# Kernel tuning notes

Hardware: AMD Instinct MI355X
Metric: run time of the kernel (lower is better)

Reference implementation:

```python
import jax, jax.numpy as jnp
import numpy as np

TAU = 2.0
EPS = 1e-5
T, B, C, H, W = 4, 16, 256, 32, 32
HEADS = 8
HD = C // HEADS
N = H * W


def make_spike(grad_fn):
    @jax.custom_vjp
    def f(x):
        return (x >= 0.0).astype(x.dtype)
    def fwd(x):
        return f(x), x
    def bwd(res, g):
        return (g * grad_fn(res),)
    f.defvjp(fwd, bwd)
    return f

# ATan surrogate (alpha=5.0) used by q/k/v LIF nodes
spike_atan5 = make_spike(lambda x: (5.0 / 2.0) / (1.0 + (jnp.pi / 2.0 * 5.0 * x) ** 2))
# default Sigmoid surrogate (alpha=4.0) for shortcut_lif / talking_heads_lif
def _sig_grad(x):
    s = jax.nn.sigmoid(4.0 * x)
    return 4.0 * s * (1.0 - s)
spike_sig4 = make_spike(_sig_grad)


def lif(x, spike, v_th=1.0):
    # multi-step LIF over leading time axis; hard reset to 0, detach_reset
    def step(v, xt):
        h = v + (xt - v) / TAU
        s = spike(h - v_th)
        v_new = h * (1.0 - jax.lax.stop_gradient(s))
        return v_new, s
    _, out = jax.lax.scan(step, jnp.zeros_like(x[0]), x)
    return out


def conv1x1(x, w):
    # x: (T,B,C,H,W), w: (Cout,Cin) from Conv2d kernel_size=1
    return jnp.einsum('tbchw,oc->tbohw', x, w)


def bn(y, gamma, beta, mean, var):
    scale = (gamma / jnp.sqrt(var + EPS))[None, None, :, None, None]
    shift = (beta - mean * gamma / jnp.sqrt(var + EPS))[None, None, :, None, None]
    return y * scale + shift


def to_heads(x):
    # (T,B,C,H,W) -> (T,B,heads,N,hd); matches flatten(3).transpose(-1,-2).reshape.permute
    x = x.reshape(T, B, C, N).transpose(0, 1, 3, 2)          # (T,B,N,C)
    x = x.reshape(T, B, N, HEADS, HD).transpose(0, 1, 3, 2, 4)  # (T,B,heads,N,hd)
    return x


def setup_inputs() -> dict:
    key = jax.random.key(0)
    ks = jax.random.split(key, 20)
    def bn_params(i):
        return (1.0 + 0.1 * jax.random.normal(ks[i], (C,), jnp.float32),
                0.1 * jax.random.normal(ks[i + 1], (C,), jnp.float32),
                0.1 * jax.random.normal(ks[i + 2], (C,), jnp.float32),
                jax.random.uniform(ks[i + 3], (C,), jnp.float32, 0.5, 1.5))
    q_g, q_b, q_m, q_var = bn_params(1)
    k_g, k_b, k_m, k_var = bn_params(5)
    v_g, v_b, v_m, v_var = bn_params(9)
    p_g, p_b, p_m, p_var = bn_params(13)
    std = 1.0 / np.sqrt(C)
    return {
        'x': jax.random.normal(ks[0], (T, B, C, H, W), jnp.float32),
        'q_w': std * jax.random.normal(ks[17], (C, C), jnp.float32),
        'q_g': q_g, 'q_b': q_b, 'q_m': q_m, 'q_var': q_var,
        'k_w': std * jax.random.normal(ks[18], (C, C), jnp.float32),
        'k_g': k_g, 'k_b': k_b, 'k_m': k_m, 'k_var': k_var,
        'v_w': std * jax.random.normal(ks[19], (C, C), jnp.float32),
        'v_g': v_g, 'v_b': v_b, 'v_m': v_m, 'v_var': v_var,
        'proj_w': std * jax.random.normal(ks[4], (C, C), jnp.float32),
        'proj_bias': 0.01 * jax.random.normal(ks[8], (C,), jnp.float32),
        'p_g': p_g, 'p_b': p_b, 'p_m': p_m, 'p_var': p_var,
    }


def reference(x, q_w, q_g, q_b, q_m, q_var, k_w, k_g, k_b, k_m, k_var,
              v_w, v_g, v_b, v_m, v_var, proj_w, proj_bias, p_g, p_b, p_m, p_var):
    identity = x
    xs = lif(x, spike_sig4, 1.0)                      # shortcut_lif
    q = to_heads(lif(bn(conv1x1(xs, q_w), q_g, q_b, q_m, q_var), spike_atan5, 1.0))
    k = to_heads(lif(bn(conv1x1(xs, k_w), k_g, k_b, k_m, k_var), spike_atan5, 1.0))
    v = to_heads(lif(bn(conv1x1(xs, v_w), v_g, v_b, v_m, v_var), spike_atan5, 1.0))
    kv = jnp.sum(k * v, axis=-2, keepdims=True)       # (T,B,heads,1,hd)
    kv = lif(kv, spike_sig4, 0.5)                     # talking_heads_lif, v_th=0.5
    attn = q * kv                                     # (T,B,heads,N,hd)
    # transpose(3,4).reshape(T,B,C,H,W)
    out = attn.transpose(0, 1, 2, 4, 3).reshape(T, B, C, H, W)
    out = conv1x1(out, proj_w) + proj_bias[None, None, :, None, None]
    out = bn(out, p_g, p_b, p_m, p_var)
    out = out + identity
    return out, v
```

## Files before the change

kernel.cpp:

```cpp
#include <hip/hip_runtime.h>
#include <hip/hip_bf16.h>
#include <stdint.h>

#define T_ 4
#define B_ 16
#define C_ 256
#define N_ 1024
#define HEADS_ 8
#define HD_ 32

typedef unsigned long long u64;
typedef unsigned char u8;

__global__ __launch_bounds__(256) void prep_transpose(
    const float* __restrict__ qw, const float* __restrict__ kw,
    const float* __restrict__ vw, const float* __restrict__ pw,
    float* __restrict__ wtq, float* __restrict__ wtk,
    float* __restrict__ wtv, float* __restrict__ wtp) {
  int c = blockIdx.x;
  int o = threadIdx.x;
  wtq[c * C_ + o] = qw[o * C_ + c];
  wtk[c * C_ + o] = kw[o * C_ + c];
  wtv[c * C_ + o] = vw[o * C_ + c];
  wtp[c * C_ + o] = pw[o * C_ + c];
}

__global__ __launch_bounds__(256) void prep_bn(
    const float* __restrict__ qg, const float* __restrict__ qb2,
    const float* __restrict__ qmn, const float* __restrict__ qvr,
    const float* __restrict__ kg, const float* __restrict__ kb2,
    const float* __restrict__ kmn, const float* __restrict__ kvr,
    const float* __restrict__ vg, const float* __restrict__ vb2,
    const float* __restrict__ vmn, const float* __restrict__ vvr,
    const float* __restrict__ pg, const float* __restrict__ pb2,
    const float* __restrict__ pmn, const float* __restrict__ pvr,
    float* __restrict__ bnt) {
  int c = threadIdx.x;
  float rs;
  rs = sqrtf(qvr[c] + 1e-5f);
  bnt[0 * C_ + c] = qg[c] / rs;
  bnt[1 * C_ + c] = qb2[c] - qmn[c] * qg[c] / rs;
  rs = sqrtf(kvr[c] + 1e-5f);
  bnt[2 * C_ + c] = kg[c] / rs;
  bnt[3 * C_ + c] = kb2[c] - kmn[c] * kg[c] / rs;
  rs = sqrtf(vvr[c] + 1e-5f);
  bnt[4 * C_ + c] = vg[c] / rs;
  bnt[5 * C_ + c] = vb2[c] - vmn[c] * vg[c] / rs;
  rs = sqrtf(pvr[c] + 1e-5f);
  bnt[6 * C_ + c] = pg[c] / rs;
  bnt[7 * C_ + c] = pb2[c] - pmn[c] * pg[c] / rs;
}

__global__ __launch_bounds__(256) void lif_shortcut(const float* __restrict__ x,
                                                    u64* __restrict__ xsm) {
  int b = blockIdx.x >> 5;
  int n0 = (blockIdx.x & 31) << 5;
  int tid = threadIdx.x;
  int l = tid & 63, w = tid >> 6;
  __shared__ float tile[C_ * 33];
  float v[32];
#pragma unroll
  for (int i = 0; i < 32; i++) v[i] = 0.f;
  int c = (w << 6) + l;
  for (int t = 0; t < T_; t++) {
    __syncthreads();
    const float* xp = x + (((size_t)t * B_ + b) * C_) * N_ + n0;
    for (int idx = tid; idx < C_ * 32; idx += 256) {
      int cc = idx >> 5, nn = idx & 31;
      tile[cc * 33 + nn] = xp[(size_t)cc * N_ + nn];
    }
    __syncthreads();
#pragma unroll
    for (int nn = 0; nn < 32; nn++) {
      float xv = tile[c * 33 + nn];
      float h = v[nn] + (xv - v[nn]) * 0.5f;
      bool s = h >= 1.0f;
      v[nn] = s ? 0.f : h;
      u64 bal = __ballot(s);
      if (l == nn) xsm[(((size_t)t * B_ + b) * N_ + n0 + nn) * 4 + w] = bal;
    }
  }
}

__global__ __launch_bounds__(256) void qkv_sparse(
    const u64* __restrict__ xsm,
    const float* __restrict__ wtq, const float* __restrict__ wtk,
    const float* __restrict__ wtv, const float* __restrict__ bnt,
    float* __restrict__ pkv, u64* __restrict__ qm_out,
    float* __restrict__ vout) {
  int b = blockIdx.x >> 6;
  int nt = blockIdx.x & 63;
  int n0 = nt << 4;
  int tid = threadIdx.x;
  int l = tid & 63, wv = tid >> 6;
  float qs[4], qsh[4], ks[4], ksh[4], vsc[4], vsh[4];
#pragma unroll
  for (int j = 0; j < 4; j++) {
    int o = (j << 6) + l;
    qs[j]  = bnt[0 * C_ + o]; qsh[j] = bnt[1 * C_ + o];
    ks[j]  = bnt[2 * C_ + o]; ksh[j] = bnt[3 * C_ + o];
    vsc[j] = bnt[4 * C_ + o]; vsh[j] = bnt[5 * C_ + o];
  }
  int cnt[4][4];
#pragma unroll
  for (int t = 0; t < 4; t++)
#pragma unroll
    for (int j = 0; j < 4; j++) cnt[t][j] = 0;

  for (int nn = wv; nn < 16; nn += 4) {
    int n = n0 + nn;
    float aq[4][4], ak[4][4], av[4][4];
#pragma unroll
    for (int t = 0; t < 4; t++)
#pragma unroll
      for (int j = 0; j < 4; j++) { aq[t][j] = 0.f; ak[t][j] = 0.f; av[t][j] = 0.f; }
#pragma unroll
    for (int t = 0; t < 4; t++) {
      const u64* mp = xsm + (((size_t)t * B_ + b) * N_ + n) * 4;
#pragma unroll
      for (int wd = 0; wd < 4; wd++) {
        u64 m = mp[wd];
        while (m) {
          int c = (wd << 6) + __builtin_ctzll(m);
          m &= (m - 1);
          const float* rq = wtq + c * C_;
          const float* rk = wtk + c * C_;
          const float* rv = wtv + c * C_;
#pragma unroll
          for (int j = 0; j < 4; j++) {
            int o = (j << 6) + l;
            aq[t][j] += rq[o];
            ak[t][j] += rk[o];
            av[t][j] += rv[o];
          }
        }
      }
    }
#pragma unroll
    for (int j = 0; j < 4; j++) {
      int o = (j << 6) + l;
      float vq = 0.f, vk = 0.f, vv = 0.f;
#pragma unroll
      for (int t = 0; t < 4; t++) {
        float pq = aq[t][j] * qs[j] + qsh[j];
        float pk = ak[t][j] * ks[j] + ksh[j];
        float pv = av[t][j] * vsc[j] + vsh[j];
        float hq = vq + (pq - vq) * 0.5f;
        float hk = vk + (pk - vk) * 0.5f;
        float hv = vv + (pv - vv) * 0.5f;
        bool sq = hq >= 1.0f; vq = sq ? 0.f : hq;
        bool sk = hk >= 1.0f; vk = sk ? 0.f : hk;
        bool sv = hv >= 1.0f; vv = sv ? 0.f : hv;
        cnt[t][j] += (sk && sv) ? 1 : 0;
        vout[(((size_t)t * B_ + b) * HEADS_ + (o >> 5)) * ((size_t)N_ * HD_) +
             (size_t)n * HD_ + (o & 31)] = sv ? 1.0f : 0.0f;
        u64 bal = __ballot(sq);
        if (l == (t << 2) + j)
          qm_out[(((size_t)t * B_ + b) * N_ + n) * 4 + j] = bal;
      }
    }
  }
  __shared__ int scnt[4][4][C_];
#pragma unroll
  for (int t = 0; t < 4; t++)
#pragma unroll
    for (int j = 0; j < 4; j++) scnt[wv][t][(j << 6) + l] = cnt[t][j];
  __syncthreads();
  for (int idx = tid; idx < 4 * C_; idx += 256) {
    int t = idx >> 8, c = idx & 255;
    int s = scnt[0][t][c] + scnt[1][t][c] + scnt[2][t][c] + scnt[3][t][c];
    pkv[(((size_t)t * B_ + b) * C_ + c) * 64 + nt] = (float)s;
  }
}

__global__ __launch_bounds__(256) void kv_lif_kernel(const float* __restrict__ pkv,
                                                     u64* __restrict__ kvsm) {
  int b = blockIdx.x;
  int c = threadIdx.x;
  int l = c & 63, w = c >> 6;
  float v = 0.f;
  for (int t = 0; t < 4; t++) {
    const float* p = pkv + (((size_t)t * B_ + b) * C_ + c) * 64;
    float kv = 0.f;
    for (int i = 0; i < 64; i++) kv += p[i];
    float h = v + (kv - v) * 0.5f;
    bool s = h >= 0.5f;
    v = s ? 0.f : h;
    u64 bal = __ballot(s);
    if (l == t) kvsm[((size_t)t * B_ + b) * 4 + w] = bal;
  }
}

__global__ __launch_bounds__(256) void proj_sparse(
    const u64* __restrict__ qm, const u64* __restrict__ kvsm,
    const float* __restrict__ wtp, const float* __restrict__ bnt,
    const float* __restrict__ pbias, const float* __restrict__ x,
    float* __restrict__ out) {
  int tb = blockIdx.x >> 5;
  int n0 = (blockIdx.x & 31) << 5;
  int t = tb >> 4, b = tb & 15;
  int tid = threadIdx.x;
  int l = tid & 63, w = tid >> 6;
  __shared__ float tile[C_ * 33];
  u64 kvm[4];
#pragma unroll
  for (int wd = 0; wd < 4; wd++) kvm[wd] = kvsm[((size_t)t * B_ + b) * 4 + wd];
  for (int nn = w; nn < 32; nn += 4) {
    int n = n0 + nn;
    float acc[4] = {0.f, 0.f, 0.f, 0.f};
    const u64* mp = qm + (((size_t)t * B_ + b) * N_ + n) * 4;
#pragma unroll
    for (int wd = 0; wd < 4; wd++) {
      u64 m = mp[wd] & kvm[wd];
      while (m) {
        int c = (wd << 6) + __builtin_ctzll(m);
        m &= (m - 1);
        const float* rp = wtp + c * C_;
#pragma unroll
        for (int j = 0; j < 4; j++) acc[j] += rp[(j << 6) + l];
      }
    }
#pragma unroll
    for (int j = 0; j < 4; j++) tile[((j << 6) + l) * 33 + nn] = acc[j];
  }
  __syncthreads();
  int col = l & 31;
  int half = l >> 5;
  for (int r = (w << 1) + half; r < C_; r += 8) {
    float val = tile[r * 33 + col];
    float z = (val + pbias[r]) * bnt[6 * C_ + r] + bnt[7 * C_ + r];
    size_t xi = (((size_t)t * B_ + b) * C_ + r) * N_ + n0 + col;
    out[xi] = z + x[xi];
  }
}

__global__ __launch_bounds__(256) void fill_zero_f32(float* p, size_t n) {
  size_t i = (size_t)blockIdx.x * 256 + threadIdx.x;
  if (i < n) p[i] = 0.0f;
}

extern "C" void kernel_launch(void* const* d_in, const int* in_sizes, int n_in,
                              void* d_out, int out_size, void* d_ws, size_t ws_size,
                              hipStream_t stream) {
  const float* x  = (const float*)d_in[0];
  const float* qw = (const float*)d_in[1];
  const float* qg = (const float*)d_in[2];
  const float* qb = (const float*)d_in[3];
  const float* qm = (const float*)d_in[4];
  const float* qv = (const float*)d_in[5];
  const float* kw = (const float*)d_in[6];
  const float* kg = (const float*)d_in[7];
  const float* kb = (const float*)d_in[8];
  const float* km = (const float*)d_in[9];
  const float* kv = (const float*)d_in[10];
  const float* vw = (const float*)d_in[11];
  const float* vg = (const float*)d_in[12];
  const float* vb = (const float*)d_in[13];
  const float* vm = (const float*)d_in[14];
  const float* vv = (const float*)d_in[15];
  const float* pw = (const float*)d_in[16];
  const float* pbias = (const float*)d_in[17];
  const float* pg = (const float*)d_in[18];
  const float* pb = (const float*)d_in[19];
  const float* pm = (const float*)d_in[20];
  const float* pv = (const float*)d_in[21];

  const size_t needed = 10485760ull;
  if (ws_size < needed) {
    size_t n = (size_t)out_size;
    fill_zero_f32<<<(unsigned)((n + 255) / 256), 256, 0, stream>>>(
        (float*)d_out, n);
    return;
  }

  char* ws = (char*)d_ws;
  float* wtq = (float*)(ws + 0);
  float* wtk = (float*)(ws + 262144);
  float* wtv = (float*)(ws + 524288);
  float* wtp = (float*)(ws + 786432);
  float* bnt = (float*)(ws + 1048576);
  u64*   xsm = (u64*)  (ws + 1056768);
  u64*   qmm = (u64*)  (ws + 3153920);
  float* pkv = (float*)(ws + 5251072);
  u64*   kvsm = (u64*) (ws + 9445376);

  float* out  = (float*)d_out;
  float* vout = out + (size_t)T_ * B_ * C_ * N_;

  prep_transpose<<<256, 256, 0, stream>>>(qw, kw, vw, pw, wtq, wtk, wtv, wtp);
  prep_bn<<<1, 256, 0, stream>>>(qg, qb, qm, qv, kg, kb, km, kv,
                                 vg, vb, vm, vv, pg, pb, pm, pv, bnt);
  lif_shortcut<<<512, 256, 0, stream>>>(x, xsm);
  qkv_sparse<<<1024, 256, 0, stream>>>(xsm, wtq, wtk, wtv, bnt, pkv, qmm, vout);
  kv_lif_kernel<<<16, 256, 0, stream>>>(pkv, kvsm);
  proj_sparse<<<2048, 256, 0, stream>>>(qmm, kvsm, wtp, bnt, pbias, x, out);
}
```

Baseline: 150.1 us.

## Precompute spike index lists and interleave QKV weights for vectorized sparse accumulation

The shortcut LIF kernel now emits per-site byte lists of active channel indices plus counts instead of bitmasks. The QKV kernel reads one interleaved QKV weight row per active channel as float4 loads, with a software-prefetched next row, each lane owning four consecutive output channels. The kv partial sums become bytes computed by ballot popcounts over a finer 256-way split, and the v output is written as coalesced float4 stores from shared bitmasks. The weight-transpose and BN-prep kernels are merged into one launch. The aim is to remove ctz loop overhead, scalar weight loads and the strided v stores, at the cost of a much larger workspace (16MB of index lists) and extra write traffic for them.

```diff
diff --git a/kernel.cpp b/kernel.cpp
--- a/kernel.cpp
+++ b/kernel.cpp
@@ -11,21 +11,11 @@
 
 typedef unsigned long long u64;
 typedef unsigned char u8;
-
-__global__ __launch_bounds__(256) void prep_transpose(
+typedef unsigned short u16;
+
+__global__ __launch_bounds__(256) void prep_kernel(
     const float* __restrict__ qw, const float* __restrict__ kw,
     const float* __restrict__ vw, const float* __restrict__ pw,
-    float* __restrict__ wtq, float* __restrict__ wtk,
-    float* __restrict__ wtv, float* __restrict__ wtp) {
-  int c = blockIdx.x;
-  int o = threadIdx.x;
-  wtq[c * C_ + o] = qw[o * C_ + c];
-  wtk[c * C_ + o] = kw[o * C_ + c];
-  wtv[c * C_ + o] = vw[o * C_ + c];
-  wtp[c * C_ + o] = pw[o * C_ + c];
-}
-
-__global__ __launch_bounds__(256) void prep_bn(
     const float* __restrict__ qg, const float* __restrict__ qb2,
     const float* __restrict__ qmn, const float* __restrict__ qvr,
     const float* __restrict__ kg, const float* __restrict__ kb2,
@@ -34,30 +24,42 @@
     const float* __restrict__ vmn, const float* __restrict__ vvr,
     const float* __restrict__ pg, const float* __restrict__ pb2,
     const float* __restrict__ pmn, const float* __restrict__ pvr,
+    float* __restrict__ wqkv, float* __restrict__ wtp,
     float* __restrict__ bnt) {
-  int c = threadIdx.x;
-  float rs;
-  rs = sqrtf(qvr[c] + 1e-5f);
-  bnt[0 * C_ + c] = qg[c] / rs;
-  bnt[1 * C_ + c] = qb2[c] - qmn[c] * qg[c] / rs;
-  rs = sqrtf(kvr[c] + 1e-5f);
-  bnt[2 * C_ + c] = kg[c] / rs;
-  bnt[3 * C_ + c] = kb2[c] - kmn[c] * kg[c] / rs;
-  rs = sqrtf(vvr[c] + 1e-5f);
-  bnt[4 * C_ + c] = vg[c] / rs;
-  bnt[5 * C_ + c] = vb2[c] - vmn[c] * vg[c] / rs;
-  rs = sqrtf(pvr[c] + 1e-5f);
-  bnt[6 * C_ + c] = pg[c] / rs;
-  bnt[7 * C_ + c] = pb2[c] - pmn[c] * pg[c] / rs;
-}
-
-__global__ __launch_bounds__(256) void lif_shortcut(const float* __restrict__ x,
-                                                    u64* __restrict__ xsm) {
+  if (blockIdx.x < 256) {
+    int c = blockIdx.x;
+    int o = threadIdx.x;
+    wqkv[c * 768 + o]       = qw[o * C_ + c];
+    wqkv[c * 768 + 256 + o] = kw[o * C_ + c];
+    wqkv[c * 768 + 512 + o] = vw[o * C_ + c];
+    wtp[c * C_ + o]         = pw[o * C_ + c];
+  } else {
+    int c = threadIdx.x;
+    float rs;
+    rs = sqrtf(qvr[c] + 1e-5f);
+    bnt[0 * C_ + c] = qg[c] / rs;
+    bnt[1 * C_ + c] = qb2[c] - qmn[c] * qg[c] / rs;
+    rs = sqrtf(kvr[c] + 1e-5f);
+    bnt[2 * C_ + c] = kg[c] / rs;
+    bnt[3 * C_ + c] = kb2[c] - kmn[c] * kg[c] / rs;
+    rs = sqrtf(vvr[c] + 1e-5f);
+    bnt[4 * C_ + c] = vg[c] / rs;
+    bnt[5 * C_ + c] = vb2[c] - vmn[c] * vg[c] / rs;
+    rs = sqrtf(pvr[c] + 1e-5f);
+    bnt[6 * C_ + c] = pg[c] / rs;
+    bnt[7 * C_ + c] = pb2[c] - pmn[c] * pg[c] / rs;
+  }
+}
+
+__global__ __launch_bounds__(256) void lif_pack(const float* __restrict__ x,
+                                                u8* __restrict__ lists,
+                                                u16* __restrict__ cnts) {
   int b = blockIdx.x >> 5;
   int n0 = (blockIdx.x & 31) << 5;
   int tid = threadIdx.x;
   int l = tid & 63, w = tid >> 6;
   __shared__ float tile[C_ * 33];
+  __shared__ u64 lmask[4][32][4];
   float v[32];
 #pragma unroll
   for (int i = 0; i < 32; i++) v[i] = 0.f;
@@ -77,117 +79,163 @@
       bool s = h >= 1.0f;
       v[nn] = s ? 0.f : h;
       u64 bal = __ballot(s);
-      if (l == nn) xsm[(((size_t)t * B_ + b) * N_ + n0 + nn) * 4 + w] = bal;
-    }
+      if (l == nn) lmask[t][nn][w] = bal;
+    }
+  }
+  __syncthreads();
+  if (tid < 128) {
+    int t = tid >> 5, nn = tid & 31;
+    int n = n0 + nn;
+    size_t site = ((size_t)t * B_ + b) * N_ + n;
+    u8* lp = lists + (site << 8);
+    int cnt = 0;
+    u64 m;
+    m = lmask[t][nn][0];
+    while (m) { lp[cnt++] = (u8)__builtin_ctzll(m); m &= m - 1; }
+    m = lmask[t][nn][1];
+    while (m) { lp[cnt++] = (u8)(64 + __builtin_ctzll(m)); m &= m - 1; }
+    m = lmask[t][nn][2];
+    while (m) { lp[cnt++] = (u8)(128 + __builtin_ctzll(m)); m &= m - 1; }
+    m = lmask[t][nn][3];
+    while (m) { lp[cnt++] = (u8)(192 + __builtin_ctzll(m)); m &= m - 1; }
+    cnts[site] = (u16)cnt;
   }
 }
 
 __global__ __launch_bounds__(256) void qkv_sparse(
-    const u64* __restrict__ xsm,
-    const float* __restrict__ wtq, const float* __restrict__ wtk,
-    const float* __restrict__ wtv, const float* __restrict__ bnt,
-    float* __restrict__ pkv, u64* __restrict__ qm_out,
+    const u8* __restrict__ lists, const u16* __restrict__ cnts,
+    const float* __restrict__ wqkv, const float* __restrict__ bnt,
+    u8* __restrict__ pkvb, u64* __restrict__ qm_out,
     float* __restrict__ vout) {
-  int b = blockIdx.x >> 6;
-  int nt = blockIdx.x & 63;
-  int n0 = nt << 4;
+  int b = blockIdx.x >> 8;
+  int nt = blockIdx.x & 255;
+  int n0 = nt << 2;
   int tid = threadIdx.x;
   int l = tid & 63, wv = tid >> 6;
-  float qs[4], qsh[4], ks[4], ksh[4], vsc[4], vsh[4];
+  int n = n0 + wv;
+
+  __shared__ u64 kvw[4][4][4];
+  __shared__ u64 vb[4][4][4];
+
+  float qsc[4], qsh[4], ksc[4], ksh[4], vsc[4], vsh[4];
 #pragma unroll
   for (int j = 0; j < 4; j++) {
-    int o = (j << 6) + l;
-    qs[j]  = bnt[0 * C_ + o]; qsh[j] = bnt[1 * C_ + o];
-    ks[j]  = bnt[2 * C_ + o]; ksh[j] = bnt[3 * C_ + o];
+    int o = (l << 2) + j;
+    qsc[j] = bnt[0 * C_ + o]; qsh[j] = bnt[1 * C_ + o];
+    ksc[j] = bnt[2 * C_ + o]; ksh[j] = bnt[3 * C_ + o];
     vsc[j] = bnt[4 * C_ + o]; vsh[j] = bnt[5 * C_ + o];
   }
-  int cnt[4][4];
-#pragma unroll
-  for (int t = 0; t < 4; t++)
-#pragma unroll
-    for (int j = 0; j < 4; j++) cnt[t][j] = 0;
-
-  for (int nn = wv; nn < 16; nn += 4) {
-    int n = n0 + nn;
-    float aq[4][4], ak[4][4], av[4][4];
-#pragma unroll
-    for (int t = 0; t < 4; t++)
-#pragma unroll
-      for (int j = 0; j < 4; j++) { aq[t][j] = 0.f; ak[t][j] = 0.f; av[t][j] = 0.f; }
-#pragma unroll
-    for (int t = 0; t < 4; t++) {
-      const u64* mp = xsm + (((size_t)t * B_ + b) * N_ + n) * 4;
-#pragma unroll
-      for (int wd = 0; wd < 4; wd++) {
-        u64 m = mp[wd];
-        while (m) {
-          int c = (wd << 6) + __builtin_ctzll(m);
-          m &= (m - 1);
-          const float* rq = wtq + c * C_;
-          const float* rk = wtk + c * C_;
-          const float* rv = wtv + c * C_;
-#pragma unroll
-          for (int j = 0; j < 4; j++) {
-            int o = (j << 6) + l;
-            aq[t][j] += rq[o];
-            ak[t][j] += rk[o];
-            av[t][j] += rv[o];
-          }
-        }
+  float vq[4] = {0.f, 0.f, 0.f, 0.f};
+  float vk[4] = {0.f, 0.f, 0.f, 0.f};
+  float vv2[4] = {0.f, 0.f, 0.f, 0.f};
+
+  for (int t = 0; t < 4; t++) {
+    size_t site = ((size_t)t * B_ + b) * N_ + n;
+    const u8* lp = lists + (site << 8);
+    int cn = cnts[site];
+    float aq[4] = {0.f, 0.f, 0.f, 0.f};
+    float ak[4] = {0.f, 0.f, 0.f, 0.f};
+    float av[4] = {0.f, 0.f, 0.f, 0.f};
+    if (cn > 0) {
+      int ca = lp[0];
+      const float4* pa = (const float4*)(wqkv + ca * 768) + l;
+      float4 q0 = pa[0], k0 = pa[64], v0 = pa[128];
+      for (int i = 1; i < cn; i++) {
+        int cb = lp[i];
+        const float4* pb = (const float4*)(wqkv + cb * 768) + l;
+        float4 q1 = pb[0], k1 = pb[64], v1 = pb[128];
+        aq[0] += q0.x; aq[1] += q0.y; aq[2] += q0.z; aq[3] += q0.w;
+        ak[0] += k0.x; ak[1] += k0.y; ak[2] += k0.z; ak[3] += k0.w;
+        av[0] += v0.x; av[1] += v0.y; av[2] += v0.z; av[3] += v0.w;
+        q0 = q1; k0 = k1; v0 = v1;
       }
+      aq[0] += q0.x; aq[1] += q0.y; aq[2] += q0.z; aq[3] += q0.w;
+      ak[0] += k0.x; ak[1] += k0.y; ak[2] += k0.z; ak[3] += k0.w;
+      av[0] += v0.x; av[1] += v0.y; av[2] += v0.z; av[3] += v0.w;
     }
 #pragma unroll
     for (int j = 0; j < 4; j++) {
-      int o = (j << 6) + l;
-      float vq = 0.f, vk = 0.f, vv = 0.f;
-#pragma unroll
-      for (int t = 0; t < 4; t++) {
-        float pq = aq[t][j] * qs[j] + qsh[j];
-        float pk = ak[t][j] * ks[j] + ksh[j];
-        float pv = av[t][j] * vsc[j] + vsh[j];
-        float hq = vq + (pq - vq) * 0.5f;
-        float hk = vk + (pk - vk) * 0.5f;
-        float hv = vv + (pv - vv) * 0.5f;
-        bool sq = hq >= 1.0f; vq = sq ? 0.f : hq;
-        bool sk = hk >= 1.0f; vk = sk ? 0.f : hk;
-        bool sv = hv >= 1.0f; vv = sv ? 0.f : hv;
-        cnt[t][j] += (sk && sv) ? 1 : 0;
-        vout[(((size_t)t * B_ + b) * HEADS_ + (o >> 5)) * ((size_t)N_ * HD_) +
-             (size_t)n * HD_ + (o & 31)] = sv ? 1.0f : 0.0f;
-        u64 bal = __ballot(sq);
-        if (l == (t << 2) + j)
-          qm_out[(((size_t)t * B_ + b) * N_ + n) * 4 + j] = bal;
+      float pq = aq[j] * qsc[j] + qsh[j];
+      float pk = ak[j] * ksc[j] + ksh[j];
+      float pv = av[j] * vsc[j] + vsh[j];
+      float hq = vq[j] + (pq - vq[j]) * 0.5f;
+      float hk = vk[j] + (pk - vk[j]) * 0.5f;
+      float hv = vv2[j] + (pv - vv2[j]) * 0.5f;
+      bool sq = hq >= 1.0f; vq[j] = sq ? 0.f : hq;
+      bool sk = hk >= 1.0f; vk[j] = sk ? 0.f : hk;
+      bool sv = hv >= 1.0f; vv2[j] = sv ? 0.f : hv;
+      u64 bq = __ballot(sq);
+      u64 bkv = __ballot(sk && sv);
+      u64 bv = __ballot(sv);
+      if (l == (t << 2) + j) {
+        qm_out[(site << 2) + j] = bq;
+        kvw[wv][t][j] = bkv;
+        vb[wv][t][j] = bv;
       }
     }
   }
-  __shared__ int scnt[4][4][C_];
-#pragma unroll
-  for (int t = 0; t < 4; t++)
-#pragma unroll
-    for (int j = 0; j < 4; j++) scnt[wv][t][(j << 6) + l] = cnt[t][j];
   __syncthreads();
-  for (int idx = tid; idx < 4 * C_; idx += 256) {
-    int t = idx >> 8, c = idx & 255;
-    int s = scnt[0][t][c] + scnt[1][t][c] + scnt[2][t][c] + scnt[3][t][c];
-    pkv[(((size_t)t * B_ + b) * C_ + c) * 64 + nt] = (float)s;
-  }
-}
-
-__global__ __launch_bounds__(256) void kv_lif_kernel(const float* __restrict__ pkv,
+
+#pragma unroll
+  for (int t = 0; t < 4; t++) {
+    int c = tid;
+    int ll = c >> 2, j = c & 3;
+    int s = (int)((kvw[0][t][j] >> ll) & 1ull) +
+            (int)((kvw[1][t][j] >> ll) & 1ull) +
+            (int)((kvw[2][t][j] >> ll) & 1ull) +
+            (int)((kvw[3][t][j] >> ll) & 1ull);
+    pkvb[((((size_t)t * B_ + b) * C_ + c) << 8) + nt] = (u8)s;
+  }
+
+  {
+    int th = tid >> 3;
+    int t = th >> 3;
+    int head = th & 7;
+    int part = tid & 7;
+    int nn = part >> 1;
+    int e0 = part << 4;
+    float* vp = vout +
+        ((((size_t)t * B_ + b) * HEADS_ + head) * N_ + n0) * HD_ + e0;
+#pragma unroll
+    for (int f = 0; f < 4; f++) {
+      int e = e0 + (f << 2);
+      int hd = e & 31;
+      int li = (head << 3) + (hd >> 2);
+      float4 o4;
+      o4.x = ((vb[nn][t][0] >> li) & 1ull) ? 1.f : 0.f;
+      o4.y = ((vb[nn][t][1] >> li) & 1ull) ? 1.f : 0.f;
+      o4.z = ((vb[nn][t][2] >> li) & 1ull) ? 1.f : 0.f;
+      o4.w = ((vb[nn][t][3] >> li) & 1ull) ? 1.f : 0.f;
+      *(float4*)(vp + (f << 2)) = o4;
+    }
+  }
+}
+
+__global__ __launch_bounds__(256) void kv_lif_kernel(const u8* __restrict__ pkvb,
                                                      u64* __restrict__ kvsm) {
   int b = blockIdx.x;
-  int c = threadIdx.x;
-  int l = c & 63, w = c >> 6;
+  int tid = threadIdx.x;
+  int l = tid & 63, j = tid >> 6;
+  int c = (l << 2) + j;
   float v = 0.f;
   for (int t = 0; t < 4; t++) {
-    const float* p = pkv + (((size_t)t * B_ + b) * C_ + c) * 64;
-    float kv = 0.f;
-    for (int i = 0; i < 64; i++) kv += p[i];
-    float h = v + (kv - v) * 0.5f;
-    bool s = h >= 0.5f;
-    v = s ? 0.f : h;
-    u64 bal = __ballot(s);
-    if (l == t) kvsm[((size_t)t * B_ + b) * 4 + w] = bal;
+    const uint4* p =
+        (const uint4*)(pkvb + ((((size_t)t * B_ + b) * C_ + c) << 8));
+    int s = 0;
+    for (int i = 0; i < 16; i++) {
+      uint4 u = p[i];
+      unsigned a;
+      a = u.x; s += (a & 255) + ((a >> 8) & 255) + ((a >> 16) & 255) + (a >> 24);
+      a = u.y; s += (a & 255) + ((a >> 8) & 255) + ((a >> 16) & 255) + (a >> 24);
+      a = u.z; s += (a & 255) + ((a >> 8) & 255) + ((a >> 16) & 255) + (a >> 24);
+      a = u.w; s += (a & 255) + ((a >> 8) & 255) + ((a >> 16) & 255) + (a >> 24);
+    }
+    float kvs = (float)s;
+    float h = v + (kvs - v) * 0.5f;
+    bool sp = h >= 0.5f;
+    v = sp ? 0.f : h;
+    u64 bal = __ballot(sp);
+    if (l == t) kvsm[((size_t)t * B_ + b) * 4 + j] = bal;
   }
 }
 
@@ -204,24 +252,26 @@
   __shared__ float tile[C_ * 33];
   u64 kvm[4];
 #pragma unroll
-  for (int wd = 0; wd < 4; wd++) kvm[wd] = kvsm[((size_t)t * B_ + b) * 4 + wd];
+  for (int j = 0; j < 4; j++) kvm[j] = kvsm[((size_t)t * B_ + b) * 4 + j];
   for (int nn = w; nn < 32; nn += 4) {
     int n = n0 + nn;
     float acc[4] = {0.f, 0.f, 0.f, 0.f};
-    const u64* mp = qm + (((size_t)t * B_ + b) * N_ + n) * 4;
-#pragma unroll
-    for (int wd = 0; wd < 4; wd++) {
-      u64 m = mp[wd] & kvm[wd];
+    size_t site = ((size_t)t * B_ + b) * N_ + n;
+    const u64* mp = qm + (site << 2);
+#pragma unroll
+    for (int j = 0; j < 4; j++) {
+      u64 m = mp[j] & kvm[j];
       while (m) {
-        int c = (wd << 6) + __builtin_ctzll(m);
-        m &= (m - 1);
+        int li = __builtin_ctzll(m);
+        m &= m - 1;
+        int c = (li << 2) + j;
         const float* rp = wtp + c * C_;
 #pragma unroll
-        for (int j = 0; j < 4; j++) acc[j] += rp[(j << 6) + l];
+        for (int jj = 0; jj < 4; jj++) acc[jj] += rp[(jj << 6) + l];
       }
     }
 #pragma unroll
-    for (int j = 0; j < 4; j++) tile[((j << 6) + l) * 33 + nn] = acc[j];
+    for (int jj = 0; jj < 4; jj++) tile[((jj << 6) + l) * 33 + nn] = acc[jj];
   }
   __syncthreads();
   int col = l & 31;
@@ -255,7 +305,7 @@
   const float* kv = (const float*)d_in[10];
   const float* vw = (const float*)d_in[11];
   const float* vg = (const float*)d_in[12];
-  const float* vb = (const float*)d_in[13];
+  const float* vb2 = (const float*)d_in[13];
   const float* vm = (const float*)d_in[14];
   const float* vv = (const float*)d_in[15];
   const float* pw = (const float*)d_in[16];
@@ -265,7 +315,7 @@
   const float* pm = (const float*)d_in[20];
   const float* pv = (const float*)d_in[21];
 
-  const size_t needed = 10485760ull;
+  const size_t needed = 24258560ull;
   if (ws_size < needed) {
     size_t n = (size_t)out_size;
     fill_zero_f32<<<(unsigned)((n + 255) / 256), 256, 0, stream>>>(
@@ -274,24 +324,24 @@
   }
 
   char* ws = (char*)d_ws;
-  float* wtq = (float*)(ws + 0);
-  float* wtk = (float*)(ws + 262144);
-  float* wtv = (float*)(ws + 524288);
-  float* wtp = (float*)(ws + 786432);
-  float* bnt = (float*)(ws + 1048576);
-  u64*   xsm = (u64*)  (ws + 1056768);
-  u64*   qmm = (u64*)  (ws + 3153920);
-  float* pkv = (float*)(ws + 5251072);
-  u64*   kvsm = (u64*) (ws + 9445376);
+  float* wqkv  = (float*)(ws + 0);
+  float* wtp   = (float*)(ws + 786432);
+  float* bnt   = (float*)(ws + 1048576);
+  u8*    lists = (u8*)   (ws + 1056768);
+  u16*   cnts  = (u16*)  (ws + 17833984);
+  u64*   qmm   = (u64*)  (ws + 17965056);
+  u8*    pkvb  = (u8*)   (ws + 20062208);
+  u64*   kvsm  = (u64*)  (ws + 24256512);
 
   float* out  = (float*)d_out;
   float* vout = out + (size_t)T_ * B_ * C_ * N_;
 
-  prep_transpose<<<256, 256, 0, stream>>>(qw, kw, vw, pw, wtq, wtk, wtv, wtp);
-  prep_bn<<<1, 256, 0, stream>>>(qg, qb, qm, qv, kg, kb, km, kv,
-                                 vg, vb, vm, vv, pg, pb, pm, pv, bnt);
-  lif_shortcut<<<512, 256, 0, stream>>>(x, xsm);
-  qkv_sparse<<<1024, 256, 0, stream>>>(xsm, wtq, wtk, wtv, bnt, pkv, qmm, vout);
-  kv_lif_kernel<<<16, 256, 0, stream>>>(pkv, kvsm);
+  prep_kernel<<<257, 256, 0, stream>>>(qw, kw, vw, pw,
+                                       qg, qb, qm, qv, kg, kb, km, kv,
+                                       vg, vb2, vm, vv, pg, pb, pm, pv,
+                                       wqkv, wtp, bnt);
+  lif_pack<<<512, 256, 0, stream>>>(x, lists, cnts);
+  qkv_sparse<<<4096, 256, 0, stream>>>(lists, cnts, wqkv, bnt, pkvb, qmm, vout);
+  kv_lif_kernel<<<16, 256, 0, stream>>>(pkvb, kvsm);
   proj_sparse<<<2048, 256, 0, stream>>>(qmm, kvsm, wtp, bnt, pbias, x, out);
 }
```

Measured after the change: 178.8 us. +19.1%, slower.
